# Performance work log

Hardware: AMD Instinct MI355X
Metric: run time of the kernel (lower is better)

Reference implementation:

```python
import jax, jax.numpy as jnp
import numpy as np

D_MODEL = 256
NUM_HEADS = 8
HEAD_DIM = D_MODEL // NUM_HEADS
B, L = 2, 2048


def setup_inputs() -> dict:
    key = jax.random.key(0)
    ks = jax.random.split(key, 16)
    s = 0.02
    return {
        "query": jax.random.normal(ks[0], (B, L, D_MODEL), jnp.float32),
        "key": jax.random.normal(ks[1], (B, L, D_MODEL), jnp.float32),
        "value": jax.random.normal(ks[2], (B, L, D_MODEL), jnp.float32),
        "struct_bias": jax.random.normal(ks[3], (B, NUM_HEADS, L, L), jnp.float32),
        "attn_mask": jax.random.normal(ks[4], (B, NUM_HEADS, L, L), jnp.float32),
        "Wq": jax.random.normal(ks[5], (D_MODEL, D_MODEL), jnp.float32) * s,
        "bq": jnp.zeros((D_MODEL,), jnp.float32),
        "Wk": jax.random.normal(ks[6], (D_MODEL, D_MODEL), jnp.float32) * s,
        "bk": jnp.zeros((D_MODEL,), jnp.float32),
        "Wv": jax.random.normal(ks[7], (D_MODEL, D_MODEL), jnp.float32) * s,
        "bv": jnp.zeros((D_MODEL,), jnp.float32),
        "Wo": jax.random.normal(ks[8], (D_MODEL, D_MODEL), jnp.float32) * s,
        "bo": jnp.zeros((D_MODEL,), jnp.float32),
    }


def reference(query, key, value, struct_bias, attn_mask,
              Wq, bq, Wk, bk, Wv, bv, Wo, bo):
    b, t, _ = query.shape
    # projections (torch Linear: x @ W.T + b)
    q = query @ Wq.T + bq
    k = key @ Wk.T + bk
    v = value @ Wv.T + bv
    # [B, H, L, Dh]
    q = q.reshape(b, t, NUM_HEADS, HEAD_DIM).transpose(0, 2, 1, 3)
    k = k.reshape(b, t, NUM_HEADS, HEAD_DIM).transpose(0, 2, 1, 3)
    v = v.reshape(b, t, NUM_HEADS, HEAD_DIM).transpose(0, 2, 1, 3)
    scale = 1.0 / np.sqrt(HEAD_DIM).astype(np.float32)
    scores = jnp.einsum("bhqd,bhkd->bhqk", q, k) * scale
    scores = scores + struct_bias + attn_mask
    attn_weights = jax.nn.softmax(scores, axis=-1)
    context = jnp.einsum("bhqk,bhkd->bhqd", attn_weights, v)
    context = context.transpose(0, 2, 1, 3).reshape(b, t, D_MODEL)
    output = context @ Wo.T + bo
    return (output, attn_weights)
```

## Files before the change

kernel.cpp:

```cpp
#include <hip/hip_runtime.h>

typedef __bf16 bf16x8 __attribute__((ext_vector_type(8)));
typedef short  s16x8  __attribute__((ext_vector_type(8)));
typedef float  f32x4  __attribute__((ext_vector_type(4)));

#define MFMA16(a,b,c) __builtin_amdgcn_mfma_f32_16x16x32_bf16((a),(b),(c),0,0,0)

static constexpr float SCALE = 0.17677669529663687f;

__device__ __forceinline__ unsigned short f2b(float f){
  __bf16 h = (__bf16)f;
  return __builtin_bit_cast(unsigned short, h);
}
__device__ __forceinline__ bf16x8 ldfrag(const unsigned short* p){
  s16x8 v = *(const s16x8*)p;
  return __builtin_bit_cast(bf16x8, v);
}
__device__ __forceinline__ bf16x8 cvt8(const float* p){
  f32x4 a = *(const f32x4*)p;
  f32x4 b = *(const f32x4*)(p+4);
  bf16x8 r;
  r[0]=(__bf16)a[0]; r[1]=(__bf16)a[1]; r[2]=(__bf16)a[2]; r[3]=(__bf16)a[3];
  r[4]=(__bf16)b[0]; r[5]=(__bf16)b[1]; r[6]=(__bf16)b[2]; r[7]=(__bf16)b[3];
  return r;
}

__global__ __launch_bounds__(256) void proj_kernel(
    const float* __restrict__ xq, const float* __restrict__ xk, const float* __restrict__ xv,
    const float* __restrict__ Wq, const float* __restrict__ bq,
    const float* __restrict__ Wk, const float* __restrict__ bk,
    const float* __restrict__ Wv, const float* __restrict__ bv,
    unsigned short* __restrict__ qo, unsigned short* __restrict__ ko,
    unsigned short* __restrict__ vT)
{
  const int z = blockIdx.z;
  const float* x    = (z==0) ? xq : (z==1 ? xk : xv);
  const float* W    = (z==0) ? Wq : (z==1 ? Wk : Wv);
  const float* bias = (z==0) ? bq : (z==1 ? bk : bv);
  const int tid = threadIdx.x, w = tid>>6, l = tid&63;
  const int m0 = blockIdx.x*16;
  const int n0 = blockIdx.y*64 + w*16;
  const int ra = l&15, ko8 = (l>>4)*8;

  f32x4 acc = {0.f,0.f,0.f,0.f};
  #pragma unroll
  for(int kk=0;kk<8;++kk){
    int kb = kk*32 + ko8;
    bf16x8 a   = cvt8(x + (m0+ra)*256 + kb);
    bf16x8 bfr = cvt8(W + (n0+ra)*256 + kb);
    acc = MFMA16(a, bfr, acc);
  }
  const int col = l&15;
  const int n = n0 + col;
  const float bval = bias[n];

  __shared__ float vt[4][16][17];
  if(z < 2){
    unsigned short* out = (z==0) ? qo : ko;
    #pragma unroll
    for(int r=0;r<4;++r){
      int R = (l>>4)*4 + r, m = m0 + R;
      float val = acc[r] + bval;
      if(z==0) val *= SCALE;
      int bidx = m>>11, ls = m&2047, hh = n>>5, dh = n&31;
      out[(((long)(bidx*8+hh))*2048 + ls)*32 + dh] = f2b(val);
    }
  } else {
    #pragma unroll
    for(int r=0;r<4;++r){
      int R = (l>>4)*4 + r;
      vt[w][R][col] = acc[r] + bval;
    }
    __syncthreads();
    int bidx = m0>>11, hh = n0>>5, dh0 = n0&31, bh = bidx*8 + hh;
    int lsc = m0 & 2047;
    int dloc = l>>2, kloc = (l&3)*4;
    ushort4 pk;
    pk.x = f2b(vt[w][kloc+0][dloc]);
    pk.y = f2b(vt[w][kloc+1][dloc]);
    pk.z = f2b(vt[w][kloc+2][dloc]);
    pk.w = f2b(vt[w][kloc+3][dloc]);
    *reinterpret_cast<ushort4*>(vT + ((long)(bh*32 + dh0 + dloc))*2048 + lsc + kloc) = pk;
  }
}

__global__ __launch_bounds__(1024) void attn_kernel(
    const unsigned short* __restrict__ qbf, const unsigned short* __restrict__ kbf,
    const unsigned short* __restrict__ vT,
    const float* __restrict__ sbias, const float* __restrict__ amask,
    float* __restrict__ Pout, float* __restrict__ ctx)
{
  __shared__ float sS[16*2048];
  __shared__ float linv[16];

  const int tid = threadIdx.x, w = tid>>6, l = tid&63;
  const int q0 = blockIdx.x*16;
  const int h = blockIdx.y, b = blockIdx.z;
  const int bh = b*8 + h;
  const long qkbase = (long)bh*2048*32;
  const long bmbase = ((long)bh*2048 + q0)*2048;
  const long rowbase = bmbase + (long)w*2048;
  const int ws = w*128;
  const int col = l&15, ko8 = (l>>4)*8, rg = (l>>4)*4;
  const f32x4 zero = {0.f,0.f,0.f,0.f};

  f32x4 s[8];
  #pragma unroll
  for(int k=0;k<8;++k){
    long c = rowbase + k*256 + l*4;
    f32x4 b4 = __builtin_nontemporal_load((const f32x4*)(sbias + c));
    f32x4 m4 = __builtin_nontemporal_load((const f32x4*)(amask + c));
    s[k] = b4 + m4;
  }

  bf16x8 aq = ldfrag(qbf + qkbase + (long)(q0+col)*32 + ko8);
  #pragma unroll
  for(int t=0;t<8;++t){
    int key0 = ws + t*16;
    bf16x8 bk = ldfrag(kbf + qkbase + (long)(key0+col)*32 + ko8);
    f32x4 acc = MFMA16(aq, bk, zero);
    #pragma unroll
    for(int r=0;r<4;++r){
      int R = rg + r;
      sS[R*2048 + ((key0+col) ^ ((R&7)<<2))] = acc[r];
    }
  }
  __syncthreads();

  const int swzw = (w&7)<<2;
  float m = -1e30f;
  #pragma unroll
  for(int k=0;k<8;++k){
    int c = k*256 + l*4;
    f32x4 v = *(const f32x4*)(&sS[w*2048 + (c ^ swzw)]);
    s[k][0]+=v[0]; s[k][1]+=v[1]; s[k][2]+=v[2]; s[k][3]+=v[3];
    m = fmaxf(m, fmaxf(fmaxf(s[k][0],s[k][1]), fmaxf(s[k][2],s[k][3])));
  }
  #pragma unroll
  for(int d=1;d<64;d<<=1) m = fmaxf(m, __shfl_xor(m, d));
  float sum = 0.f;
  #pragma unroll
  for(int k=0;k<8;++k){
    s[k][0]=__expf(s[k][0]-m); s[k][1]=__expf(s[k][1]-m);
    s[k][2]=__expf(s[k][2]-m); s[k][3]=__expf(s[k][3]-m);
    sum += (s[k][0]+s[k][1]) + (s[k][2]+s[k][3]);
  }
  #pragma unroll
  for(int d=1;d<64;d<<=1) sum += __shfl_xor(sum, d);
  const float li = 1.0f/sum;
  if(l==0) linv[w] = li;

  #pragma unroll
  for(int k=0;k<8;++k){
    int c = k*256 + l*4;
    f32x4 p; p[0]=s[k][0]*li; p[1]=s[k][1]*li; p[2]=s[k][2]*li; p[3]=s[k][3]*li;
    __builtin_nontemporal_store(p, (f32x4*)(Pout + rowbase + c));
    *(f32x4*)(&sS[w*2048 + (c ^ swzw)]) = s[k];
  }
  __syncthreads();

  f32x4 acc0 = zero, acc1 = zero;
  const long vbase = (long)bh*32*2048;
  #pragma unroll
  for(int c=0;c<4;++c){
    int kb = ws + c*32 + ko8;
    f32x4 e0 = *(const f32x4*)(&sS[col*2048 + ( kb    ^ ((col&7)<<2))]);
    f32x4 e1 = *(const f32x4*)(&sS[col*2048 + ((kb+4) ^ ((col&7)<<2))]);
    bf16x8 pa;
    pa[0]=(__bf16)e0[0]; pa[1]=(__bf16)e0[1]; pa[2]=(__bf16)e0[2]; pa[3]=(__bf16)e0[3];
    pa[4]=(__bf16)e1[0]; pa[5]=(__bf16)e1[1]; pa[6]=(__bf16)e1[2]; pa[7]=(__bf16)e1[3];
    bf16x8 v0 = ldfrag(vT + vbase + (long)col*2048 + kb);
    bf16x8 v1 = ldfrag(vT + vbase + (long)(16+col)*2048 + kb);
    acc0 = MFMA16(pa, v0, acc0);
    acc1 = MFMA16(pa, v1, acc1);
  }
  __syncthreads();

  #pragma unroll
  for(int r=0;r<4;++r){
    int R = rg + r;
    sS[w*512 + R*32 + col]      = acc0[r];
    sS[w*512 + R*32 + 16 + col] = acc1[r];
  }
  __syncthreads();
  if(tid < 512){
    int row = tid>>5, dh = tid&31;
    float ssum = 0.f;
    #pragma unroll
    for(int w2=0; w2<16; ++w2) ssum += sS[w2*512 + row*32 + dh];
    ctx[((long)b*2048 + q0 + row)*256 + h*32 + dh] = ssum * linv[row];
  }
}

__global__ __launch_bounds__(256) void oproj_kernel(
    float* __restrict__ out0, const float* __restrict__ Wo, const float* __restrict__ bo)
{
  __shared__ float lct[16*260];
  const int tid = threadIdx.x, w = tid>>6, l = tid&63;
  const int m0 = blockIdx.x*16;
  #pragma unroll
  for(int i=0;i<4;++i){
    int idx = tid + i*256;
    int row = idx>>6, c4 = (idx&63)*4;
    *(f32x4*)(&lct[row*260 + c4]) = *(const f32x4*)(out0 + (m0+row)*256 + c4);
  }
  __syncthreads();
  const int col = l&15, ko8 = (l>>4)*8, rg = (l>>4)*4;
  #pragma unroll
  for(int nt=0;nt<4;++nt){
    int n0 = w*64 + nt*16;
    f32x4 acc = {0.f,0.f,0.f,0.f};
    #pragma unroll
    for(int kk=0;kk<8;++kk){
      int kb = kk*32 + ko8;
      bf16x8 a   = cvt8(&lct[col*260 + kb]);
      bf16x8 bfr = cvt8(Wo + (n0+col)*256 + kb);
      acc = MFMA16(a, bfr, acc);
    }
    float bv = bo[n0+col];
    #pragma unroll
    for(int r=0;r<4;++r){
      out0[(m0+rg+r)*256 + n0+col] = acc[r] + bv;
    }
  }
}

extern "C" void kernel_launch(void* const* d_in, const int* in_sizes, int n_in,
                              void* d_out, int out_size, void* d_ws, size_t ws_size,
                              hipStream_t stream)
{
  const float* query = (const float*)d_in[0];
  const float* key   = (const float*)d_in[1];
  const float* value = (const float*)d_in[2];
  const float* sbias = (const float*)d_in[3];
  const float* amask = (const float*)d_in[4];
  const float* Wq = (const float*)d_in[5];
  const float* bq = (const float*)d_in[6];
  const float* Wk = (const float*)d_in[7];
  const float* bk = (const float*)d_in[8];
  const float* Wv = (const float*)d_in[9];
  const float* bv = (const float*)d_in[10];
  const float* Wo = (const float*)d_in[11];
  const float* bo = (const float*)d_in[12];

  float* out0 = (float*)d_out;
  float* Pout = out0 + (size_t)2*2048*256;

  unsigned short* qbf = (unsigned short*)d_ws;
  unsigned short* kbf = qbf + (size_t)2*8*2048*32;
  unsigned short* vTb = kbf + (size_t)2*8*2048*32;

  proj_kernel<<<dim3(256,4,3), 256, 0, stream>>>(query,key,value,Wq,bq,Wk,bk,Wv,bv,qbf,kbf,vTb);
  attn_kernel<<<dim3(128,8,2), 1024, 0, stream>>>(qbf,kbf,vTb,sbias,amask,Pout,out0);
  oproj_kernel<<<dim3(256), 256, 0, stream>>>(out0,Wo,bo);
}
```

Measured before the change: 222.8 us.

## Halve attention query tile to 8 rows and stage bf16 activations in LDS

The attention kernel now processes 8 query rows per block with 512 threads instead of 16 rows with 1024, which halves its LDS footprint to 64KB and doubles the grid. This should let more blocks fit per CU and improve latency hiding on a kernel that mostly streams the large bias and mask tensors. In exchange, each MFMA computes 16 rows and half are discarded, and each wave now covers twice as many keys. The projection and output-projection kernels convert their activation tile to bf16 once into shared memory rather than reconverting it on every fragment load, and the output projection also moves to 8-row tiles.

```diff
diff --git a/kernel.cpp b/kernel.cpp
--- a/kernel.cpp
+++ b/kernel.cpp
@@ -42,11 +42,22 @@
   const int n0 = blockIdx.y*64 + w*16;
   const int ra = l&15, ko8 = (l>>4)*8;
 
+  __shared__ unsigned short xs[16*264];
+  #pragma unroll
+  for(int i=0;i<4;++i){
+    int chunk = tid + i*256;
+    int row = chunk>>6, c4 = (chunk&63)*4;
+    f32x4 v = *(const f32x4*)(x + (m0+row)*256 + c4);
+    ushort4 u; u.x=f2b(v[0]); u.y=f2b(v[1]); u.z=f2b(v[2]); u.w=f2b(v[3]);
+    *(ushort4*)(&xs[row*264 + c4]) = u;
+  }
+  __syncthreads();
+
   f32x4 acc = {0.f,0.f,0.f,0.f};
   #pragma unroll
   for(int kk=0;kk<8;++kk){
     int kb = kk*32 + ko8;
-    bf16x8 a   = cvt8(x + (m0+ra)*256 + kb);
+    bf16x8 a   = ldfrag(&xs[ra*264 + kb]);
     bf16x8 bfr = cvt8(W + (n0+ra)*256 + kb);
     acc = MFMA16(a, bfr, acc);
   }
@@ -84,23 +95,23 @@
   }
 }
 
-__global__ __launch_bounds__(1024) void attn_kernel(
+__global__ __launch_bounds__(512) void attn_kernel(
     const unsigned short* __restrict__ qbf, const unsigned short* __restrict__ kbf,
     const unsigned short* __restrict__ vT,
     const float* __restrict__ sbias, const float* __restrict__ amask,
     float* __restrict__ Pout, float* __restrict__ ctx)
 {
-  __shared__ float sS[16*2048];
-  __shared__ float linv[16];
+  __shared__ float sS[8*2048];
+  __shared__ float linv[8];
 
   const int tid = threadIdx.x, w = tid>>6, l = tid&63;
-  const int q0 = blockIdx.x*16;
+  const int q0 = blockIdx.x*8;
   const int h = blockIdx.y, b = blockIdx.z;
   const int bh = b*8 + h;
   const long qkbase = (long)bh*2048*32;
   const long bmbase = ((long)bh*2048 + q0)*2048;
   const long rowbase = bmbase + (long)w*2048;
-  const int ws = w*128;
+  const int ws = w*256;
   const int col = l&15, ko8 = (l>>4)*8, rg = (l>>4)*4;
   const f32x4 zero = {0.f,0.f,0.f,0.f};
 
@@ -113,21 +124,23 @@
     s[k] = b4 + m4;
   }
 
-  bf16x8 aq = ldfrag(qbf + qkbase + (long)(q0+col)*32 + ko8);
-  #pragma unroll
-  for(int t=0;t<8;++t){
+  bf16x8 aq = ldfrag(qbf + qkbase + (long)(q0 + (col&7))*32 + ko8);
+  #pragma unroll
+  for(int t=0;t<16;++t){
     int key0 = ws + t*16;
     bf16x8 bk = ldfrag(kbf + qkbase + (long)(key0+col)*32 + ko8);
     f32x4 acc = MFMA16(aq, bk, zero);
-    #pragma unroll
-    for(int r=0;r<4;++r){
-      int R = rg + r;
-      sS[R*2048 + ((key0+col) ^ ((R&7)<<2))] = acc[r];
-    }
-  }
-  __syncthreads();
-
-  const int swzw = (w&7)<<2;
+    if(rg < 8){
+      #pragma unroll
+      for(int r=0;r<4;++r){
+        int R = rg + r;
+        sS[R*2048 + ((key0+col) ^ (R<<2))] = acc[r];
+      }
+    }
+  }
+  __syncthreads();
+
+  const int swzw = w<<2;
   float m = -1e30f;
   #pragma unroll
   for(int k=0;k<8;++k){
@@ -161,11 +174,12 @@
 
   f32x4 acc0 = zero, acc1 = zero;
   const long vbase = (long)bh*32*2048;
-  #pragma unroll
-  for(int c=0;c<4;++c){
+  const int prow = col&7;
+  #pragma unroll
+  for(int c=0;c<8;++c){
     int kb = ws + c*32 + ko8;
-    f32x4 e0 = *(const f32x4*)(&sS[col*2048 + ( kb    ^ ((col&7)<<2))]);
-    f32x4 e1 = *(const f32x4*)(&sS[col*2048 + ((kb+4) ^ ((col&7)<<2))]);
+    f32x4 e0 = *(const f32x4*)(&sS[prow*2048 + ( kb    ^ (prow<<2))]);
+    f32x4 e1 = *(const f32x4*)(&sS[prow*2048 + ((kb+4) ^ (prow<<2))]);
     bf16x8 pa;
     pa[0]=(__bf16)e0[0]; pa[1]=(__bf16)e0[1]; pa[2]=(__bf16)e0[2]; pa[3]=(__bf16)e0[3];
     pa[4]=(__bf16)e1[0]; pa[5]=(__bf16)e1[1]; pa[6]=(__bf16)e1[2]; pa[7]=(__bf16)e1[3];
@@ -176,18 +190,20 @@
   }
   __syncthreads();
 
-  #pragma unroll
-  for(int r=0;r<4;++r){
-    int R = rg + r;
-    sS[w*512 + R*32 + col]      = acc0[r];
-    sS[w*512 + R*32 + 16 + col] = acc1[r];
-  }
-  __syncthreads();
-  if(tid < 512){
+  if(rg < 8){
+    #pragma unroll
+    for(int r=0;r<4;++r){
+      int R = rg + r;
+      sS[w*256 + R*32 + col]      = acc0[r];
+      sS[w*256 + R*32 + 16 + col] = acc1[r];
+    }
+  }
+  __syncthreads();
+  if(tid < 256){
     int row = tid>>5, dh = tid&31;
     float ssum = 0.f;
     #pragma unroll
-    for(int w2=0; w2<16; ++w2) ssum += sS[w2*512 + row*32 + dh];
+    for(int w2=0; w2<8; ++w2) ssum += sS[w2*256 + row*32 + dh];
     ctx[((long)b*2048 + q0 + row)*256 + h*32 + dh] = ssum * linv[row];
   }
 }
@@ -195,17 +211,20 @@
 __global__ __launch_bounds__(256) void oproj_kernel(
     float* __restrict__ out0, const float* __restrict__ Wo, const float* __restrict__ bo)
 {
-  __shared__ float lct[16*260];
+  __shared__ unsigned short lct[8*264];
   const int tid = threadIdx.x, w = tid>>6, l = tid&63;
-  const int m0 = blockIdx.x*16;
-  #pragma unroll
-  for(int i=0;i<4;++i){
-    int idx = tid + i*256;
-    int row = idx>>6, c4 = (idx&63)*4;
-    *(f32x4*)(&lct[row*260 + c4]) = *(const f32x4*)(out0 + (m0+row)*256 + c4);
+  const int m0 = blockIdx.x*8;
+  #pragma unroll
+  for(int i=0;i<2;++i){
+    int chunk = tid + i*256;
+    int row = chunk>>6, c4 = (chunk&63)*4;
+    f32x4 v = *(const f32x4*)(out0 + (m0+row)*256 + c4);
+    ushort4 u; u.x=f2b(v[0]); u.y=f2b(v[1]); u.z=f2b(v[2]); u.w=f2b(v[3]);
+    *(ushort4*)(&lct[row*264 + c4]) = u;
   }
   __syncthreads();
   const int col = l&15, ko8 = (l>>4)*8, rg = (l>>4)*4;
+  const int arow = col&7;
   #pragma unroll
   for(int nt=0;nt<4;++nt){
     int n0 = w*64 + nt*16;
@@ -213,14 +232,16 @@
     #pragma unroll
     for(int kk=0;kk<8;++kk){
       int kb = kk*32 + ko8;
-      bf16x8 a   = cvt8(&lct[col*260 + kb]);
+      bf16x8 a   = ldfrag(&lct[arow*264 + kb]);
       bf16x8 bfr = cvt8(Wo + (n0+col)*256 + kb);
       acc = MFMA16(a, bfr, acc);
     }
     float bv = bo[n0+col];
-    #pragma unroll
-    for(int r=0;r<4;++r){
-      out0[(m0+rg+r)*256 + n0+col] = acc[r] + bv;
+    if(rg < 8){
+      #pragma unroll
+      for(int r=0;r<4;++r){
+        out0[(m0+rg+r)*256 + n0+col] = acc[r] + bv;
+      }
     }
   }
 }
@@ -251,6 +272,6 @@
   unsigned short* vTb = kbf + (size_t)2*8*2048*32;
 
   proj_kernel<<<dim3(256,4,3), 256, 0, stream>>>(query,key,value,Wq,bq,Wk,bk,Wv,bv,qbf,kbf,vTb);
-  attn_kernel<<<dim3(128,8,2), 1024, 0, stream>>>(qbf,kbf,vTb,sbias,amask,Pout,out0);
-  oproj_kernel<<<dim3(256), 256, 0, stream>>>(out0,Wo,bo);
-}
+  attn_kernel<<<dim3(256,8,2), 512, 0, stream>>>(qbf,kbf,vTb,sbias,amask,Pout,out0);
+  oproj_kernel<<<dim3(512), 256, 0, stream>>>(out0,Wo,bo);
+}
```

Measured after the change: 244.4 us. 9.7% more time.
